# Performance work log

Hardware: AMD Instinct MI355X
Metric: run time of the kernel (lower is better)

## Reference

```python
import jax, jax.numpy as jnp
import numpy as np

N_NODES = 20000
N_EDGES = 640000
IN_DIM = 128
HID = 128
NUM_GRAPHS = 64


def setup_inputs() -> dict:
    key = jax.random.key(0)
    ks = jax.random.split(key, 12)
    x = jax.random.normal(ks[0], (N_NODES, IN_DIM), dtype=jnp.float32)
    edge_index = jax.random.randint(ks[1], (2, N_EDGES), 0, N_NODES, dtype=jnp.int64)
    batch = jnp.sort(jax.random.randint(ks[2], (N_NODES,), 0, NUM_GRAPHS, dtype=jnp.int64))
    edge_attr = jax.random.uniform(ks[3], (N_EDGES,), dtype=jnp.float32)
    s1 = 1.0 / np.sqrt(IN_DIM)
    s2 = 1.0 / np.sqrt(HID)
    # GraphConv layer 1: lin_rel (with bias) on aggregated messages, lin_root (no bias) on x
    W1_rel = jax.random.uniform(ks[4], (HID, IN_DIM), minval=-s1, maxval=s1, dtype=jnp.float32)
    b1 = jax.random.uniform(ks[5], (HID,), minval=-s1, maxval=s1, dtype=jnp.float32)
    W1_root = jax.random.uniform(ks[6], (HID, IN_DIM), minval=-s1, maxval=s1, dtype=jnp.float32)
    # GraphConv layer 3 (conv2 is unused in forward)
    W3_rel = jax.random.uniform(ks[7], (HID, HID), minval=-s2, maxval=s2, dtype=jnp.float32)
    b3 = jax.random.uniform(ks[8], (HID,), minval=-s2, maxval=s2, dtype=jnp.float32)
    W3_root = jax.random.uniform(ks[9], (HID, HID), minval=-s2, maxval=s2, dtype=jnp.float32)
    # Final linear head
    Wlin = jax.random.uniform(ks[10], (1, HID), minval=-s2, maxval=s2, dtype=jnp.float32)
    blin = jax.random.uniform(ks[11], (1,), minval=-s2, maxval=s2, dtype=jnp.float32)
    return {
        "x": x, "edge_index": edge_index, "batch": batch, "edge_attr": edge_attr,
        "W1_rel": W1_rel, "b1": b1, "W1_root": W1_root,
        "W3_rel": W3_rel, "b3": b3, "W3_root": W3_root,
        "Wlin": Wlin, "blin": blin, "num_graphs": NUM_GRAPHS,
    }


def graph_conv(x, src, dst, edge_w, W_rel, b_rel, W_root):
    # PyG GraphConv (aggr='add'): out = W_rel @ sum_{j in N(i)} w_ij * x_j + b_rel + W_root @ x_i
    msg = x[src] * edge_w[:, None]                       # [E, d] gather + scale
    agg = jax.ops.segment_sum(msg, dst, num_segments=x.shape[0])  # [N, d] scatter-add
    return agg @ W_rel.T + b_rel + x @ W_root.T


def reference(x, edge_index, batch, edge_attr,
              W1_rel, b1, W1_root, W3_rel, b3, W3_root, Wlin, blin, num_graphs):
    src, dst = edge_index[0], edge_index[1]
    h = graph_conv(x, src, dst, edge_attr, W1_rel, b1, W1_root)
    h = jax.nn.relu(h)
    # dropout p=0.5 is identity in eval mode
    h = graph_conv(h, src, dst, edge_attr, W3_rel, b3, W3_root)
    # global_mean_pool over per-node graph ids
    sums = jax.ops.segment_sum(h, batch, num_segments=num_graphs)          # [G, H]
    counts = jax.ops.segment_sum(jnp.ones((h.shape[0],), h.dtype), batch,
                                 num_segments=num_graphs)                  # [G]
    pooled = sums / jnp.maximum(counts, 1.0)[:, None]
    out = jax.nn.relu(pooled @ Wlin.T + blin)                              # [G, 1]
    return out
```

## Files before the change

### kernel.cpp

```cpp
#include <hip/hip_runtime.h>

#define N_NODES 20000
#define N_EDGES 640000
#define DIM 128
#define NGRAPH 64
#define NBUCK 313
#define EPB 2048
#define NB_CONV 256
#define NB_HIST 313
#define NB_WCONV 32
#define NB_GEMM 313
#define RED_BLOCKS 512

typedef __attribute__((ext_vector_type(8))) short short8;
typedef __attribute__((ext_vector_type(4))) float floatx4;

__device__ __forceinline__ unsigned int bf16rne(float f) {
    unsigned int u = __float_as_uint(f);
    return (u + 0x7FFFu + ((u >> 16) & 1u)) >> 16;
}

__global__ __launch_bounds__(256) void k_front(
    const float* __restrict__ x, const int* __restrict__ dst,
    const float* __restrict__ Wrel, const float* __restrict__ Wroot,
    const float* __restrict__ W3rel, const float* __restrict__ W3root,
    const float* __restrict__ b3, const float* __restrict__ Wlin,
    unsigned short* __restrict__ xbh, unsigned short* __restrict__ xbl,
    unsigned short* __restrict__ wbh, unsigned short* __restrict__ wbl,
    int* __restrict__ ghist, int* __restrict__ ticket_hist,
    int* __restrict__ boff, int* __restrict__ gcursor,
    float* __restrict__ vrel, float* __restrict__ vroot, float* __restrict__ cb3) {

    const int t = threadIdx.x;
    const int blk = blockIdx.x;

    if (blk < NB_CONV) {
        const float4* x4 = (const float4*)x;
        uint2* xh2 = (uint2*)xbh;
        uint2* xl2 = (uint2*)xbl;
        for (int i = blk * 256 + t; i < N_NODES * 32; i += NB_CONV * 256) {
            float4 v = x4[i];
            unsigned int h0 = bf16rne(v.x), h1 = bf16rne(v.y);
            unsigned int h2 = bf16rne(v.z), h3 = bf16rne(v.w);
            float l0 = v.x - __uint_as_float(h0 << 16);
            float l1 = v.y - __uint_as_float(h1 << 16);
            float l2 = v.z - __uint_as_float(h2 << 16);
            float l3 = v.w - __uint_as_float(h3 << 16);
            uint2 hp, lp;
            hp.x = h0 | (h1 << 16);
            hp.y = h2 | (h3 << 16);
            lp.x = bf16rne(l0) | (bf16rne(l1) << 16);
            lp.y = bf16rne(l2) | (bf16rne(l3) << 16);
            xh2[i] = hp;
            xl2[i] = lp;
        }
    } else if (blk < NB_CONV + NB_HIST) {
        __shared__ int lhist[NBUCK];
        __shared__ int islast;
        const int hb = blk - NB_CONV;
        for (int i = t; i < NBUCK; i += 256) lhist[i] = 0;
        __syncthreads();
        const int e0 = hb * EPB;
        for (int i = 0; i < 8; ++i) {
            int e = e0 + i * 256 + t;
            if (e < N_EDGES) atomicAdd(&lhist[dst[e] >> 6], 1);
        }
        __syncthreads();
        for (int i = t; i < NBUCK; i += 256)
            if (lhist[i]) atomicAdd(&ghist[i], lhist[i]);
        __syncthreads();
        if (t == 0) {
            __threadfence();
            islast = (atomicAdd(ticket_hist, 1) == NB_HIST - 1);
        }
        __syncthreads();
        if (islast) {
            __threadfence();
            if (t < 64) {
                int carry = 0;
                for (int c = 0; c < 5; ++c) {
                    int idx = c * 64 + t;
                    int v = (idx < NBUCK)
                        ? __hip_atomic_load(&ghist[idx], __ATOMIC_RELAXED,
                                            __HIP_MEMORY_SCOPE_AGENT)
                        : 0;
                    int xv = v;
                    for (int s = 1; s < 64; s <<= 1) {
                        int u = __shfl_up(xv, s);
                        if (t >= s) xv += u;
                    }
                    int excl = carry + xv - v;
                    if (idx < NBUCK) { boff[idx] = excl; gcursor[idx] = excl; }
                    carry += __shfl(xv, 63);
                }
                if (t == 0) boff[NBUCK] = carry;
            }
        }
    } else if (blk < NB_CONV + NB_HIST + NB_WCONV) {
        const int b = blk - (NB_CONV + NB_HIST);
        for (int i = b * 256 + t; i < 256 * DIM; i += NB_WCONV * 256) {
            int n = i >> 7, k = i & 127;
            float v = (n < DIM) ? Wrel[n * DIM + k] : Wroot[(n - DIM) * DIM + k];
            unsigned int h = bf16rne(v);
            wbh[i] = (unsigned short)h;
            wbl[i] = (unsigned short)bf16rne(v - __uint_as_float(h << 16));
        }
    } else {
        if (t < 64) {
            for (int kk = 0; kk < 2; ++kk) {
                int k = t + kk * 64;
                float sr = 0.f, so = 0.f;
                for (int h = 0; h < DIM; ++h) {
                    float wl = Wlin[h];
                    sr = fmaf(wl, W3rel[h * DIM + k], sr);
                    so = fmaf(wl, W3root[h * DIM + k], so);
                }
                vrel[k] = sr;
                vroot[k] = so;
            }
            float c = b3[t] * Wlin[t] + b3[t + 64] * Wlin[t + 64];
            for (int m = 32; m > 0; m >>= 1) c += __shfl_xor(c, m);
            if (t == 0) cb3[0] = c;
        }
    }
}

__global__ __launch_bounds__(256) void k_mid(
    const int* __restrict__ src, const int* __restrict__ dst,
    const float* __restrict__ ew,
    int* __restrict__ gcursor, int2* __restrict__ part,
    const unsigned short* __restrict__ xbh, const unsigned short* __restrict__ xbl,
    const unsigned short* __restrict__ wbh, const unsigned short* __restrict__ wbl,
    const float* __restrict__ b1,
    unsigned short* __restrict__ yb, float* __restrict__ r) {

    const int t = threadIdx.x;
    if (blockIdx.x < NB_HIST) {
        __shared__ int lhist[NBUCK], gbase[NBUCK], lcur[NBUCK];
        for (int i = t; i < NBUCK; i += 256) lhist[i] = 0;
        __syncthreads();
        const int e0 = blockIdx.x * EPB;
        int mys[8], myd[8];
        float myw[8];
        for (int i = 0; i < 8; ++i) {
            int e = e0 + i * 256 + t;
            if (e < N_EDGES) {
                mys[i] = src[e];
                myd[i] = dst[e];
                myw[i] = ew[e];
                atomicAdd(&lhist[myd[i] >> 6], 1);
            } else {
                myd[i] = -1;
            }
        }
        __syncthreads();
        for (int i = t; i < NBUCK; i += 256) {
            gbase[i] = lhist[i] ? atomicAdd(&gcursor[i], lhist[i]) : 0;
            lcur[i] = 0;
        }
        __syncthreads();
        for (int i = 0; i < 8; ++i) {
            if (myd[i] >= 0) {
                int b = myd[i] >> 6;
                int rk = atomicAdd(&lcur[b], 1);
                part[gbase[b] + rk] =
                    make_int2(((myd[i] & 63) << 16) | mys[i], __float_as_int(myw[i]));
            }
        }
    } else {
        const int g = blockIdx.x - NB_HIST;
        const int lane = t & 63;
        const int m = lane & 15;
        const int q = lane >> 4;
        const int row0 = g * 64 + (t >> 6) * 16;

        const short8* Ah = (const short8*)xbh;
        const short8* Al = (const short8*)xbl;
        const short8* Bh = (const short8*)wbh;
        const short8* Bl = (const short8*)wbl;
        const int arow = (row0 + m) * 16 + q;

        floatx4 acc[16];
        #pragma unroll
        for (int i = 0; i < 16; ++i) acc[i] = (floatx4)(0.f);

        #pragma unroll
        for (int kc = 0; kc < 4; ++kc) {
            short8 ah = Ah[arow + kc * 4];
            short8 al = Al[arow + kc * 4];
            #pragma unroll
            for (int nt = 0; nt < 16; ++nt) {
                int bidx = (nt * 16 + m) * 16 + kc * 4 + q;
                short8 bh = Bh[bidx];
                short8 bl = Bl[bidx];
                acc[nt] = __builtin_amdgcn_mfma_f32_16x16x32_bf16(ah, bh, acc[nt], 0, 0, 0);
                acc[nt] = __builtin_amdgcn_mfma_f32_16x16x32_bf16(al, bh, acc[nt], 0, 0, 0);
                acc[nt] = __builtin_amdgcn_mfma_f32_16x16x32_bf16(ah, bl, acc[nt], 0, 0, 0);
            }
        }

        #pragma unroll
        for (int nt = 0; nt < 16; ++nt) {
            int col = nt * 16 + m;
            float bias = (col >= DIM) ? b1[col - DIM] : 0.f;
            #pragma unroll
            for (int reg = 0; reg < 4; ++reg) {
                int row = row0 + q * 4 + reg;
                if (row < N_NODES) {
                    float v = acc[nt][reg];
                    if (col < DIM)
                        yb[row * DIM + col] = (unsigned short)bf16rne(v);
                    else
                        r[row * DIM + (col - DIM)] = v + bias;
                }
            }
        }
    }
}

__global__ __launch_bounds__(256) void k_bucketsort(const int* __restrict__ boff,
                                                    const int2* __restrict__ part,
                                                    int2* __restrict__ sorted,
                                                    int* __restrict__ off) {
    __shared__ int nh[64], ncur[64];
    const int b = blockIdx.x;
    const int t = threadIdx.x;
    const int s0 = boff[b], s1 = boff[b + 1];
    if (t < 64) nh[t] = 0;
    __syncthreads();
    for (int i = s0 + t; i < s1; i += 256) atomicAdd(&nh[part[i].x >> 16], 1);
    __syncthreads();
    if (t < 64) {
        int v = nh[t];
        int xv = v;
        for (int s = 1; s < 64; s <<= 1) {
            int u = __shfl_up(xv, s);
            if (t >= s) xv += u;
        }
        int excl = xv - v;
        ncur[t] = excl;
        int node = b * 64 + t;
        if (node < N_NODES) off[node] = s0 + excl;
    }
    __syncthreads();
    for (int i = s0 + t; i < s1; i += 256) {
        int2 rc = part[i];
        int dl = rc.x >> 16;
        int p = atomicAdd(&ncur[dl], 1);
        sorted[s0 + p] = make_int2(rc.x & 0xFFFF, rc.y);
    }
    if (b == 0 && t == 0) off[N_NODES] = N_EDGES;
}

__global__ __launch_bounds__(256) void k_agg(const unsigned int* __restrict__ yb,
                                             const float2* __restrict__ r2,
                                             const int* __restrict__ off,
                                             const int2* __restrict__ grec,
                                             const float2* __restrict__ vrel2,
                                             const float2* __restrict__ vroot2,
                                             float* __restrict__ aout,
                                             float* __restrict__ bout) {
    const int lane = threadIdx.x & 63;
    const int node = blockIdx.x * 4 + (threadIdx.x >> 6);
    if (node >= N_NODES) return;

    int j = off[node];
    const int e1 = off[node + 1];
    float sx = 0.f, sy = 0.f;
    for (; j + 4 <= e1; j += 4) {
        int2 r0 = grec[j], r1 = grec[j + 1], rr2 = grec[j + 2], r3 = grec[j + 3];
        float w0 = __int_as_float(r0.y), w1 = __int_as_float(r1.y);
        float w2 = __int_as_float(rr2.y), w3 = __int_as_float(r3.y);
        unsigned int v0 = yb[r0.x * 64 + lane];
        unsigned int v1 = yb[r1.x * 64 + lane];
        unsigned int v2 = yb[rr2.x * 64 + lane];
        unsigned int v3 = yb[r3.x * 64 + lane];
        sx = fmaf(w0, __uint_as_float(v0 << 16),
             fmaf(w1, __uint_as_float(v1 << 16),
             fmaf(w2, __uint_as_float(v2 << 16),
             fmaf(w3, __uint_as_float(v3 << 16), sx))));
        sy = fmaf(w0, __uint_as_float(v0 & 0xFFFF0000u),
             fmaf(w1, __uint_as_float(v1 & 0xFFFF0000u),
             fmaf(w2, __uint_as_float(v2 & 0xFFFF0000u),
             fmaf(w3, __uint_as_float(v3 & 0xFFFF0000u), sy))));
    }
    for (; j < e1; ++j) {
        int2 rc = grec[j];
        float w = __int_as_float(rc.y);
        unsigned int v = yb[rc.x * 64 + lane];
        sx = fmaf(w, __uint_as_float(v << 16), sx);
        sy = fmaf(w, __uint_as_float(v & 0xFFFF0000u), sy);
    }
    float2 rr = r2[node * 64 + lane];
    float hx = fmaxf(sx + rr.x, 0.f);
    float hy = fmaxf(sy + rr.y, 0.f);
    float2 vr = vrel2[lane];
    float2 vo = vroot2[lane];
    float pa = hx * vr.x + hy * vr.y;
    float pb = hx * vo.x + hy * vo.y;
    for (int mm = 32; mm > 0; mm >>= 1) {
        pa += __shfl_xor(pa, mm);
        pb += __shfl_xor(pb, mm);
    }
    if (lane == 0) {
        aout[node] = pa;
        bout[node] = pb;
    }
}

__global__ __launch_bounds__(256) void k_reduce_final(
    const int2* __restrict__ sorted, const int* __restrict__ off,
    const float* __restrict__ a, const float* __restrict__ bvec,
    const int* __restrict__ batch,
    float* __restrict__ gpart, int* __restrict__ gpartc,
    int* __restrict__ ticket_red,
    const float* __restrict__ cb3, const float* __restrict__ blin,
    float* __restrict__ out) {
    __shared__ float sbin[NGRAPH];
    __shared__ int cbin[NGRAPH];
    __shared__ int islast;
    const int t = threadIdx.x;
    for (int i = t; i < NGRAPH; i += 256) { sbin[i] = 0.f; cbin[i] = 0; }
    __syncthreads();
    const int lane = t & 63;
    const int gw = blockIdx.x * 4 + (t >> 6);
    const int nw = gridDim.x * 4;
    for (int node = gw; node < N_NODES; node += nw) {
        const int e0 = off[node], e1 = off[node + 1];
        float s = 0.f;
        for (int j = e0 + lane; j < e1; j += 64) {
            int2 rc = sorted[j];
            s = fmaf(__int_as_float(rc.y), a[rc.x], s);
        }
        for (int mm = 32; mm > 0; mm >>= 1) s += __shfl_xor(s, mm);
        if (lane == 0) {
            int g = batch[node];
            atomicAdd(&sbin[g], s + bvec[node]);
            atomicAdd(&cbin[g], 1);
        }
    }
    __syncthreads();
    const int slot = blockIdx.x & 63;
    for (int i = t; i < NGRAPH; i += 256) {
        atomicAdd(&gpart[slot * NGRAPH + i], sbin[i]);
        if (cbin[i]) atomicAdd(&gpartc[slot * NGRAPH + i], cbin[i]);
    }
    __syncthreads();
    if (t == 0) {
        __threadfence();
        islast = (atomicAdd(ticket_red, 1) == (int)gridDim.x - 1);
    }
    __syncthreads();
    if (islast) {
        __threadfence();
        if (t < NGRAPH) {
            float S = 0.f;
            int C = 0;
            for (int s2 = 0; s2 < 64; ++s2) {
                S += __hip_atomic_load(&gpart[s2 * NGRAPH + t], __ATOMIC_RELAXED,
                                       __HIP_MEMORY_SCOPE_AGENT);
                C += __hip_atomic_load(&gpartc[s2 * NGRAPH + t], __ATOMIC_RELAXED,
                                       __HIP_MEMORY_SCOPE_AGENT);
            }
            float denom = (C > 0) ? (float)C : 1.f;
            float v = (S + (float)C * cb3[0]) / denom + blin[0];
            out[t] = (v > 0.f) ? v : 0.f;
        }
    }
}

extern "C" void kernel_launch(void* const* d_in, const int* in_sizes, int n_in,
                              void* d_out, int out_size, void* d_ws, size_t ws_size,
                              hipStream_t stream) {
    const float* x = (const float*)d_in[0];
    const int* edge_index = (const int*)d_in[1];
    const int* src = edge_index;
    const int* dst = edge_index + N_EDGES;
    const int* batch = (const int*)d_in[2];
    const float* ew = (const float*)d_in[3];
    const float* W1rel = (const float*)d_in[4];
    const float* b1 = (const float*)d_in[5];
    const float* W1root = (const float*)d_in[6];
    const float* W3rel = (const float*)d_in[7];
    const float* b3 = (const float*)d_in[8];
    const float* W3root = (const float*)d_in[9];
    const float* Wlin = (const float*)d_in[10];
    const float* blin = (const float*)d_in[11];
    float* out = (float*)d_out;

    char* w = (char*)d_ws;
    size_t o = 0;
    auto alloc = [&](size_t bytes) -> void* {
        void* p = w + o;
        o += bytes;
        o = (o + 255) & ~(size_t)255;
        return p;
    };
    char* zbase = (char*)alloc(1280 + 64 * NGRAPH * 4 * 2);
    int* ghist = (int*)zbase;
    int* ticket_hist = ghist + NBUCK;
    int* ticket_red = ghist + NBUCK + 1;
    float* gpart = (float*)(zbase + 1280);
    int* gpartc = (int*)(zbase + 1280 + 64 * NGRAPH * 4);
    const size_t zbytes = 1280 + 64 * NGRAPH * 4 * 2;

    unsigned short* xbh = (unsigned short*)alloc((size_t)20032 * DIM * 2);
    unsigned short* xbl = (unsigned short*)alloc((size_t)20032 * DIM * 2);
    unsigned short* wbh = (unsigned short*)alloc((size_t)256 * DIM * 2);
    unsigned short* wbl = (unsigned short*)alloc((size_t)256 * DIM * 2);
    unsigned short* yb = (unsigned short*)alloc((size_t)N_NODES * DIM * 2);
    float* r = (float*)alloc((size_t)N_NODES * DIM * 4);
    int* boff = (int*)alloc((size_t)(NBUCK + 1) * 4);
    int* gcursor = (int*)alloc((size_t)NBUCK * 4);
    int2* part = (int2*)alloc((size_t)N_EDGES * 8);
    int2* sorted = (int2*)alloc((size_t)N_EDGES * 8);
    int* off = (int*)alloc((size_t)(N_NODES + 1) * 4);
    float* a = (float*)alloc((size_t)N_NODES * 4);
    float* b = (float*)alloc((size_t)N_NODES * 4);
    float* vrel = (float*)alloc(DIM * 4);
    float* vroot = (float*)alloc(DIM * 4);
    float* cb3 = (float*)alloc(4);

    hipMemsetAsync(zbase, 0, zbytes, stream);

    k_front<<<NB_CONV + NB_HIST + NB_WCONV + 1, 256, 0, stream>>>(
        x, dst, W1rel, W1root, W3rel, W3root, b3, Wlin,
        xbh, xbl, wbh, wbl, ghist, ticket_hist, boff, gcursor,
        vrel, vroot, cb3);

    k_mid<<<NB_HIST + NB_GEMM, 256, 0, stream>>>(
        src, dst, ew, gcursor, part, xbh, xbl, wbh, wbl, b1, yb, r);

    k_bucketsort<<<NBUCK, 256, 0, stream>>>(boff, part, sorted, off);

    k_agg<<<(N_NODES + 3) / 4, 256, 0, stream>>>(
        (const unsigned int*)yb, (const float2*)r, off, sorted,
        (const float2*)vrel, (const float2*)vroot, a, b);

    k_reduce_final<<<RED_BLOCKS, 256, 0, stream>>>(
        sorted, off, a, b, batch, gpart, gpartc, ticket_red, cb3, blin, out);
}
```

Measured before the change: 207.1 us.

## Split fused partition/GEMM kernel and stage GEMM weights in swizzled LDS

The combined k_mid kernel is split into a separate edge-partition kernel and a GEMM kernel. The GEMM now runs on a 2D grid where each block handles half of the 256 output columns and stages the hi/lo bf16 weight halves in 64 KB of XOR-swizzled shared memory, instead of reading weights from global memory in the inner loop. This should cut global/L2 traffic for the weights and halve per-block accumulator registers. The costs are an extra kernel launch, the loss of concurrency between partition and GEMM blocks, A tiles being loaded twice, and 64 KB of LDS per block limiting occupancy.

```diff
diff --git a/kernel.cpp b/kernel.cpp
--- a/kernel.cpp
+++ b/kernel.cpp
@@ -9,7 +9,6 @@
 #define NB_CONV 256
 #define NB_HIST 313
 #define NB_WCONV 32
-#define NB_GEMM 313
 #define RED_BLOCKS 512
 
 typedef __attribute__((ext_vector_type(8))) short short8;
@@ -125,94 +124,113 @@
     }
 }
 
-__global__ __launch_bounds__(256) void k_mid(
-    const int* __restrict__ src, const int* __restrict__ dst,
-    const float* __restrict__ ew,
-    int* __restrict__ gcursor, int2* __restrict__ part,
+__global__ __launch_bounds__(256) void k_partition(const int* __restrict__ src,
+                                                   const int* __restrict__ dst,
+                                                   const float* __restrict__ ew,
+                                                   int* __restrict__ gcursor,
+                                                   int2* __restrict__ part) {
+    __shared__ int lhist[NBUCK], gbase[NBUCK], lcur[NBUCK];
+    const int t = threadIdx.x;
+    for (int i = t; i < NBUCK; i += 256) lhist[i] = 0;
+    __syncthreads();
+    const int e0 = blockIdx.x * EPB;
+    int mys[8], myd[8];
+    float myw[8];
+    for (int i = 0; i < 8; ++i) {
+        int e = e0 + i * 256 + t;
+        if (e < N_EDGES) {
+            mys[i] = src[e];
+            myd[i] = dst[e];
+            myw[i] = ew[e];
+            atomicAdd(&lhist[myd[i] >> 6], 1);
+        } else {
+            myd[i] = -1;
+        }
+    }
+    __syncthreads();
+    for (int i = t; i < NBUCK; i += 256) {
+        gbase[i] = lhist[i] ? atomicAdd(&gcursor[i], lhist[i]) : 0;
+        lcur[i] = 0;
+    }
+    __syncthreads();
+    for (int i = 0; i < 8; ++i) {
+        if (myd[i] >= 0) {
+            int b = myd[i] >> 6;
+            int rk = atomicAdd(&lcur[b], 1);
+            part[gbase[b] + rk] =
+                make_int2(((myd[i] & 63) << 16) | mys[i], __float_as_int(myw[i]));
+        }
+    }
+}
+
+__global__ __launch_bounds__(256) void k_gemm(
     const unsigned short* __restrict__ xbh, const unsigned short* __restrict__ xbl,
     const unsigned short* __restrict__ wbh, const unsigned short* __restrict__ wbl,
     const float* __restrict__ b1,
     unsigned short* __restrict__ yb, float* __restrict__ r) {
+    extern __shared__ unsigned short smem[];
+    uint4* sh = (uint4*)smem;
+    uint4* sl = (uint4*)(smem + 16384);
 
     const int t = threadIdx.x;
-    if (blockIdx.x < NB_HIST) {
-        __shared__ int lhist[NBUCK], gbase[NBUCK], lcur[NBUCK];
-        for (int i = t; i < NBUCK; i += 256) lhist[i] = 0;
-        __syncthreads();
-        const int e0 = blockIdx.x * EPB;
-        int mys[8], myd[8];
-        float myw[8];
-        for (int i = 0; i < 8; ++i) {
-            int e = e0 + i * 256 + t;
-            if (e < N_EDGES) {
-                mys[i] = src[e];
-                myd[i] = dst[e];
-                myw[i] = ew[e];
-                atomicAdd(&lhist[myd[i] >> 6], 1);
-            } else {
-                myd[i] = -1;
-            }
-        }
-        __syncthreads();
-        for (int i = t; i < NBUCK; i += 256) {
-            gbase[i] = lhist[i] ? atomicAdd(&gcursor[i], lhist[i]) : 0;
-            lcur[i] = 0;
-        }
-        __syncthreads();
-        for (int i = 0; i < 8; ++i) {
-            if (myd[i] >= 0) {
-                int b = myd[i] >> 6;
-                int rk = atomicAdd(&lcur[b], 1);
-                part[gbase[b] + rk] =
-                    make_int2(((myd[i] & 63) << 16) | mys[i], __float_as_int(myw[i]));
-            }
-        }
-    } else {
-        const int g = blockIdx.x - NB_HIST;
-        const int lane = t & 63;
-        const int m = lane & 15;
-        const int q = lane >> 4;
-        const int row0 = g * 64 + (t >> 6) * 16;
-
-        const short8* Ah = (const short8*)xbh;
-        const short8* Al = (const short8*)xbl;
-        const short8* Bh = (const short8*)wbh;
-        const short8* Bl = (const short8*)wbl;
-        const int arow = (row0 + m) * 16 + q;
-
-        floatx4 acc[16];
+    const int g = blockIdx.x;
+    const int half = blockIdx.y;
+    const int n0 = half * 128;
+
+    const uint4* gh = (const uint4*)wbh + (size_t)n0 * 16;
+    const uint4* gl = (const uint4*)wbl + (size_t)n0 * 16;
+    for (int i = t; i < 2048; i += 256) {
+        int row = i >> 4, c = i & 15;
+        int sc = row * 16 + (c ^ (row & 15));
+        sh[sc] = gh[i];
+        sl[sc] = gl[i];
+    }
+    __syncthreads();
+
+    const int lane = t & 63;
+    const int m = lane & 15;
+    const int q = lane >> 4;
+    const int row0 = g * 64 + (t >> 6) * 16;
+    const int arow = (row0 + m) * 16 + q;
+
+    const short8* Ah = (const short8*)xbh;
+    const short8* Al = (const short8*)xbl;
+    const short8* SH = (const short8*)smem;
+    const short8* SL = (const short8*)(smem + 16384);
+
+    floatx4 acc[8];
+    #pragma unroll
+    for (int i = 0; i < 8; ++i) acc[i] = (floatx4)(0.f);
+
+    #pragma unroll
+    for (int kc = 0; kc < 4; ++kc) {
+        short8 ah = Ah[arow + kc * 4];
+        short8 al = Al[arow + kc * 4];
         #pragma unroll
-        for (int i = 0; i < 16; ++i) acc[i] = (floatx4)(0.f);
-
+        for (int nt = 0; nt < 8; ++nt) {
+            int n = nt * 16 + m;
+            int cc = (kc * 4 + q) ^ m;
+            short8 bh = SH[n * 16 + cc];
+            short8 bl = SL[n * 16 + cc];
+            acc[nt] = __builtin_amdgcn_mfma_f32_16x16x32_bf16(ah, bh, acc[nt], 0, 0, 0);
+            acc[nt] = __builtin_amdgcn_mfma_f32_16x16x32_bf16(al, bh, acc[nt], 0, 0, 0);
+            acc[nt] = __builtin_amdgcn_mfma_f32_16x16x32_bf16(ah, bl, acc[nt], 0, 0, 0);
+        }
+    }
+
+    #pragma unroll
+    for (int nt = 0; nt < 8; ++nt) {
+        int col = n0 + nt * 16 + m;
+        float bias = (col >= DIM) ? b1[col - DIM] : 0.f;
         #pragma unroll
-        for (int kc = 0; kc < 4; ++kc) {
-            short8 ah = Ah[arow + kc * 4];
-            short8 al = Al[arow + kc * 4];
-            #pragma unroll
-            for (int nt = 0; nt < 16; ++nt) {
-                int bidx = (nt * 16 + m) * 16 + kc * 4 + q;
-                short8 bh = Bh[bidx];
-                short8 bl = Bl[bidx];
-                acc[nt] = __builtin_amdgcn_mfma_f32_16x16x32_bf16(ah, bh, acc[nt], 0, 0, 0);
-                acc[nt] = __builtin_amdgcn_mfma_f32_16x16x32_bf16(al, bh, acc[nt], 0, 0, 0);
-                acc[nt] = __builtin_amdgcn_mfma_f32_16x16x32_bf16(ah, bl, acc[nt], 0, 0, 0);
-            }
-        }
-
-        #pragma unroll
-        for (int nt = 0; nt < 16; ++nt) {
-            int col = nt * 16 + m;
-            float bias = (col >= DIM) ? b1[col - DIM] : 0.f;
-            #pragma unroll
-            for (int reg = 0; reg < 4; ++reg) {
-                int row = row0 + q * 4 + reg;
-                if (row < N_NODES) {
-                    float v = acc[nt][reg];
-                    if (col < DIM)
-                        yb[row * DIM + col] = (unsigned short)bf16rne(v);
-                    else
-                        r[row * DIM + (col - DIM)] = v + bias;
-                }
+        for (int reg = 0; reg < 4; ++reg) {
+            int row = row0 + q * 4 + reg;
+            if (row < N_NODES) {
+                float v = acc[nt][reg];
+                if (col < DIM)
+                    yb[row * DIM + col] = (unsigned short)bf16rne(v);
+                else
+                    r[row * DIM + (col - DIM)] = v + bias;
             }
         }
     }
@@ -428,8 +446,10 @@
         xbh, xbl, wbh, wbl, ghist, ticket_hist, boff, gcursor,
         vrel, vroot, cb3);
 
-    k_mid<<<NB_HIST + NB_GEMM, 256, 0, stream>>>(
-        src, dst, ew, gcursor, part, xbh, xbl, wbh, wbl, b1, yb, r);
+    k_partition<<<NB_HIST, 256, 0, stream>>>(src, dst, ew, gcursor, part);
+
+    k_gemm<<<dim3(NBUCK, 2), 256, 65536, stream>>>(
+        xbh, xbl, wbh, wbl, b1, yb, r);
 
     k_bucketsort<<<NBUCK, 256, 0, stream>>>(boff, part, sorted, off);
 
```

Result: faster. 196.1 us (-5.3%).
